# Kernel optimization log

Hardware: AMD Instinct MI355X
Metric: run time of the kernel (lower is better)

## Reference

```python
import jax, jax.numpy as jnp
import numpy as np


def setup_inputs() -> dict:
    key = jax.random.key(0)
    k1, k2, k3 = jax.random.split(key, 3)
    B, N, M, C = 4, 4096, 8192, 64
    PPU = 64.0  # points_per_unit
    xz = jax.random.normal(k1, (B, M, 1), dtype=jnp.float32) * 10.0  # grid locations
    z = jax.random.normal(k2, (B, C, M), dtype=jnp.float32)          # channels-first features
    x = jax.random.normal(k3, (B, N, 1), dtype=jnp.float32) * 10.0   # query locations
    log_scale = jnp.asarray(np.log(2.0 / PPU), dtype=jnp.float32)
    return {"xz": xz, "z": z, "x": x, "log_scale": log_scale}


def reference(xz, z, x, log_scale):
    # pairwise squared distances between x [B,N,1] and xz [B,M,1] -> [B,N,M]
    diff = x - jnp.swapaxes(xz, -1, -2)            # [B,N,M]
    dists2 = diff * diff
    # RBF weights (no normalization)
    weights = jnp.exp(-0.5 * dists2 / jnp.exp(2.0 * log_scale))  # [B,N,M]
    # z: [B,C,M] -> transpose -> [B,M,C]; weights @ z^T -> [B,N,C]
    out = jnp.einsum('bnm,bcm->bnc', weights, z)
    return out
```

## Files before the change

### kernel.cpp

```cpp
#include <hip/hip_runtime.h>
#include <math.h>

#define B 4
#define N 4096
#define M 8192
#define C 64
#define NB 2048
#define XMIN (-64.0f)
#define INV_BW 16.0f
#define CUT 10.0f
#define QG 16
#define NSUBP 4
#define NSUBQ 2

typedef __attribute__((ext_vector_type(8))) short short8;
typedef __attribute__((ext_vector_type(4))) float f32x4;

__device__ __forceinline__ int bucket_of(float v) {
    int k = (int)floorf((v - XMIN) * INV_BW);
    return min(max(k, 0), NB - 1);
}

__device__ __forceinline__ unsigned short f2bf(float f) {
    unsigned int u = __float_as_uint(f);
    return (unsigned short)((u + 0x7FFF + ((u >> 16) & 1)) >> 16);
}

__global__ __launch_bounds__(1024) void prep_kernel(
    const float* __restrict__ xz, const float* __restrict__ x,
    const float* __restrict__ z,
    int* __restrict__ part,
    unsigned short* __restrict__ zt)
{
    const int t   = threadIdx.x;
    const int blk = blockIdx.x;

    __shared__ int   h[NB];
    __shared__ float tile[64][65];

    if (blk < 24) {
        h[t] = 0; h[t + 1024] = 0;
        __syncthreads();
        const bool isQ = blk >= 16;
        const int  b   = isQ ? (blk - 16) >> 1 : blk >> 2;
        const int  sub = isQ ? (blk - 16) & 1  : blk & 3;
        const float* src = (isQ ? x + b * N : xz + b * M) + sub * 2048;
        float2 v2 = *(const float2*)(src + t * 2);
        atomicAdd(&h[bucket_of(v2.x)], 1);
        atomicAdd(&h[bucket_of(v2.y)], 1);
        __syncthreads();
        part[blk * NB + t]        = h[t];
        part[blk * NB + 1024 + t] = h[1024 + t];
    } else {
        const int tix = blk - 24;
        const int b   = tix >> 7;
        const int m0  = (tix & 127) * 64;
        const int m   = t & 63;
        #pragma unroll
        for (int k = 0; k < 4; ++k) {
            int c = (t >> 6) + 16 * k;
            tile[c][m] = z[((size_t)b * C + c) * M + m0 + m];
        }
        __syncthreads();
        const int j  = t >> 4;
        const int c4 = t & 15;
        ushort4 v4;
        v4.x = f2bf(tile[c4 * 4 + 0][j]);
        v4.y = f2bf(tile[c4 * 4 + 1][j]);
        v4.z = f2bf(tile[c4 * 4 + 2][j]);
        v4.w = f2bf(tile[c4 * 4 + 3][j]);
        ((ushort4*)zt)[((size_t)b * M + m0 + j) * 16 + c4] = v4;
    }
}

__global__ __launch_bounds__(256) void scat_kernel(
    const float* __restrict__ xz, const float* __restrict__ x,
    const int* __restrict__ part,
    int* __restrict__ bucket_start,
    float* __restrict__ xs,
    int* __restrict__ iord,
    float* __restrict__ qcs,
    int* __restrict__ qis)
{
    const int t    = threadIdx.x;
    const int lane = t & 63;
    const int w    = t >> 6;
    const int bid  = blockIdx.x;
    const bool isQ = bid >= 16;
    const int  b   = isQ ? (bid - 16) >> 1 : bid >> 2;
    const int  sub = isQ ? (bid - 16) & 1  : bid & 3;
    const int  nsub = isQ ? NSUBQ : NSUBP;
    const int  pb0  = isQ ? 16 + b * 2 : b * 4;
    const float* src = (isQ ? x + b * N : xz + b * M) + sub * 2048;

    __shared__ int base[NB];
    __shared__ int cnt[NB];
    __shared__ int wsum[4];

    int tot[8], mine[8];
    #pragma unroll
    for (int j = 0; j < 8; ++j) { tot[j] = 0; mine[j] = 0; }
    for (int s_ = 0; s_ < nsub; ++s_) {
        #pragma unroll
        for (int j = 0; j < 8; ++j) {
            const int v = part[(pb0 + s_) * NB + t * 8 + j];
            tot[j] += v;
            if (s_ < sub) mine[j] += v;
        }
    }
    int pre[8]; int tsum = 0;
    #pragma unroll
    for (int j = 0; j < 8; ++j) { pre[j] = tsum; tsum += tot[j]; }
    int s = tsum;
    #pragma unroll
    for (int off = 1; off < 64; off <<= 1) {
        int up = __shfl_up(s, off, 64);
        if (lane >= off) s += up;
    }
    if (lane == 63) wsum[w] = s;
    #pragma unroll
    for (int i = 0; i < 8; ++i) cnt[t + 256 * i] = 0;
    __syncthreads();
    int woff = 0;
    for (int i = 0; i < w; ++i) woff += wsum[i];
    const int excl = woff + s - tsum;
    #pragma unroll
    for (int j = 0; j < 8; ++j) base[t * 8 + j] = excl + pre[j] + mine[j];
    if (!isQ && sub == 0) {
        #pragma unroll
        for (int j = 0; j < 8; ++j)
            bucket_start[b * (NB + 1) + t * 8 + j] = excl + pre[j];
        if (t == 255) bucket_start[b * (NB + 1) + NB] = woff + s;
    }
    __syncthreads();

    #pragma unroll
    for (int j = 0; j < 2; ++j) {
        float4 v4 = *(const float4*)(src + t * 4 + j * 1024);
        float vv[4] = {v4.x, v4.y, v4.z, v4.w};
        #pragma unroll
        for (int c = 0; c < 4; ++c) {
            const int k    = bucket_of(vv[c]);
            const int slot = base[k] + atomicAdd(&cnt[k], 1);
            const int orig = sub * 2048 + t * 4 + j * 1024 + c;
            if (!isQ) {
                xs[b * M + slot]   = vv[c];
                iord[b * M + slot] = orig;
            } else {
                qcs[b * N + slot] = vv[c];
                qis[b * N + slot] = orig;
            }
        }
    }
}

__global__ __launch_bounds__(256) void gather_kernel(
    const float* __restrict__ log_scale,
    const int* __restrict__ bucket_start,
    const float* __restrict__ xs,
    const float* __restrict__ qcs,
    const int* __restrict__ qis,
    const int* __restrict__ iord,
    const unsigned short* __restrict__ zt,
    float* __restrict__ out)
{
    const int t    = threadIdx.x;
    const int lane = t & 63;
    const int w    = t >> 6;
    const int quad = lane >> 4;
    const int low4 = lane & 15;
    const int g  = blockIdx.x;
    const int b  = g >> 8;
    const int g0 = (g & 255) * QG;

    __shared__ unsigned short zr[64 * 64];
    __shared__ unsigned short wl[QG][72];
    __shared__ float qcS[QG];
    __shared__ int   qiS[QG];

    const float ls   = log_scale[0];
    const float coef = -0.5f * __expf(-2.0f * ls);
    const float R    = sqrtf(CUT / (-coef));

    if (t < QG) {
        qcS[t] = qcs[b * N + g0 + t];
        qiS[t] = qis[b * N + g0 + t];
    }
    __syncthreads();

    float xmin = qcS[0], xmax = qcS[0];
    #pragma unroll
    for (int j = 1; j < QG; ++j) {
        xmin = fminf(xmin, qcS[j]);
        xmax = fmaxf(xmax, qcS[j]);
    }
    const int s0 = bucket_start[b * (NB + 1) + bucket_of(xmin - R)];
    const int s1 = bucket_start[b * (NB + 1) + bucket_of(xmax + R) + 1];
    const int e0 = s0 & ~63;
    const int e1 = (s1 + 63) & ~63;

    const int qw = w * 4 + (lane >> 4);
    const int pg = lane & 15;
    const float qv = qcS[qw];

    f32x4 acc = {0.f, 0.f, 0.f, 0.f};

    const float* xsb = xs + b * M;
    const int* iordb = iord + b * M;
    const unsigned short* ztb = zt + (size_t)b * M * C;

    for (int cs = e0; cs < e1; cs += 64) {
        __syncthreads();
        #pragma unroll
        for (int r = 0; r < 2; ++r) {
            const int ridx = (w * 2 + r) * 8 + (lane >> 3);
            const int gm   = iordb[cs + ridx];
            const unsigned short* gp = ztb + (size_t)gm * C + (lane & 7) * 8;
            unsigned short* lp = zr + (w * 2 + r) * 512;
            __builtin_amdgcn_global_load_lds(
                (const __attribute__((address_space(1))) void*)gp,
                (__attribute__((address_space(3))) void*)lp, 16, 0, 0);
        }
        {
            const float4 xp4 = *(const float4*)(xsb + cs + pg * 4);
            float d0 = qv - xp4.x, d1 = qv - xp4.y;
            float d2 = qv - xp4.z, d3 = qv - xp4.w;
            ushort4 wv;
            wv.x = f2bf(__expf(coef * d0 * d0));
            wv.y = f2bf(__expf(coef * d1 * d1));
            wv.z = f2bf(__expf(coef * d2 * d2));
            wv.w = f2bf(__expf(coef * d3 * d3));
            *(ushort4*)&wl[qw][pg * 4] = wv;
        }
        __syncthreads();
        #pragma unroll
        for (int kh = 0; kh < 2; ++kh) {
            short8 afrag = *(const short8*)&wl[low4][kh * 32 + quad * 8];
            short8 bfrag;
            #pragma unroll
            for (int j = 0; j < 8; ++j) {
                const int p = kh * 32 + quad * 8 + j;
                bfrag[j] = (short)zr[p * 64 + w * 16 + low4];
            }
            acc = __builtin_amdgcn_mfma_f32_16x16x32_bf16(afrag, bfrag, acc, 0, 0, 0);
        }
    }

    #pragma unroll
    for (int r = 0; r < 4; ++r) {
        const int q = quad * 4 + r;
        out[((size_t)b * N + qiS[q]) * C + w * 16 + low4] = acc[r];
    }
}

extern "C" void kernel_launch(void* const* d_in, const int* in_sizes, int n_in,
                              void* d_out, int out_size, void* d_ws, size_t ws_size,
                              hipStream_t stream) {
    const float* xz = (const float*)d_in[0];
    const float* z  = (const float*)d_in[1];
    const float* x  = (const float*)d_in[2];
    const float* ls = (const float*)d_in[3];
    float* out = (float*)d_out;

    char* ws = (char*)d_ws;
    size_t off = 0;
    auto alloc = [&](size_t bytes) { void* p = ws + off; off += (bytes + 255) & ~size_t(255); return p; };

    unsigned short* zt = (unsigned short*)alloc((size_t)B * M * C * sizeof(unsigned short));
    float* xs   = (float*)alloc(((size_t)B * M + 64) * sizeof(float));
    int*   iord = (int*)alloc((size_t)B * M * sizeof(int));
    float* qcs  = (float*)alloc((size_t)B * N * sizeof(float));
    int*   qis  = (int*)alloc((size_t)B * N * sizeof(int));
    int*   bst  = (int*)alloc((size_t)B * (NB + 1) * sizeof(int));
    int*   part = (int*)alloc((size_t)24 * NB * sizeof(int));

    prep_kernel<<<536, 1024, 0, stream>>>(xz, x, z, part, zt);
    scat_kernel<<<24, 256, 0, stream>>>(xz, x, part, bst, xs, iord, qcs, qis);
    gather_kernel<<<B * (N / QG), 256, 0, stream>>>(ls, bst, xs, qcs, qis, iord, zt, out);
}
```

Measured before the change: 82.45 us.

## Prefetch next chunk's grid indices and positions; compute query range from sorted endpoints

Software-pipelines the per-chunk loads of grid indices and grid coordinates one iteration ahead, so the dependent gather address and the weight computation no longer wait on a global load at the top of each iteration. It also computes the query range from the first and last sorted query coordinates straight from global memory, before the first barrier, rather than scanning shared memory after a barrier. The bucket range is widened by one bucket on each side as a safety margin, which can add chunks of work. The new range logic assumes the queries are sorted within each group.

```diff
diff --git a/kernel.cpp b/kernel.cpp
--- a/kernel.cpp
+++ b/kernel.cpp
@@ -186,51 +186,66 @@
         qcS[t] = qcs[b * N + g0 + t];
         qiS[t] = qis[b * N + g0 + t];
     }
-    __syncthreads();
-
-    float xmin = qcS[0], xmax = qcS[0];
-    #pragma unroll
-    for (int j = 1; j < QG; ++j) {
-        xmin = fminf(xmin, qcS[j]);
-        xmax = fmaxf(xmax, qcS[j]);
-    }
-    const int s0 = bucket_start[b * (NB + 1) + bucket_of(xmin - R)];
-    const int s1 = bucket_start[b * (NB + 1) + bucket_of(xmax + R) + 1];
+
+    const float qlo = qcs[b * N + g0];
+    const float qhi = qcs[b * N + g0 + QG - 1];
+    const int k0 = max(bucket_of(qlo - R) - 1, 0);
+    const int k1 = min(bucket_of(qhi + R) + 1, NB - 1);
+    const int s0 = bucket_start[b * (NB + 1) + k0];
+    const int s1 = bucket_start[b * (NB + 1) + k1 + 1];
     const int e0 = s0 & ~63;
     const int e1 = (s1 + 63) & ~63;
 
-    const int qw = w * 4 + (lane >> 4);
-    const int pg = lane & 15;
-    const float qv = qcS[qw];
-
-    f32x4 acc = {0.f, 0.f, 0.f, 0.f};
+    const int qw = w * 4 + quad;
+    const int pg = low4;
 
     const float* xsb = xs + b * M;
     const int* iordb = iord + b * M;
     const unsigned short* ztb = zt + (size_t)b * M * C;
 
+    const int ridx0 = (w * 2 + 0) * 8 + (lane >> 3);
+    const int ridx1 = (w * 2 + 1) * 8 + (lane >> 3);
+    int gmA = 0, gmB = 0;
+    float4 xpA = {0.f, 0.f, 0.f, 0.f};
+    if (e0 < e1) {
+        gmA = iordb[e0 + ridx0];
+        gmB = iordb[e0 + ridx1];
+        xpA = *(const float4*)(xsb + e0 + pg * 4);
+    }
+
+    __syncthreads();
+    const float qv = qcS[qw];
+
+    f32x4 acc = {0.f, 0.f, 0.f, 0.f};
+
     for (int cs = e0; cs < e1; cs += 64) {
         __syncthreads();
-        #pragma unroll
-        for (int r = 0; r < 2; ++r) {
-            const int ridx = (w * 2 + r) * 8 + (lane >> 3);
-            const int gm   = iordb[cs + ridx];
-            const unsigned short* gp = ztb + (size_t)gm * C + (lane & 7) * 8;
-            unsigned short* lp = zr + (w * 2 + r) * 512;
+        {
+            const unsigned short* gpA = ztb + (size_t)gmA * C + (lane & 7) * 8;
+            const unsigned short* gpB = ztb + (size_t)gmB * C + (lane & 7) * 8;
             __builtin_amdgcn_global_load_lds(
-                (const __attribute__((address_space(1))) void*)gp,
-                (__attribute__((address_space(3))) void*)lp, 16, 0, 0);
+                (const __attribute__((address_space(1))) void*)gpA,
+                (__attribute__((address_space(3))) void*)(zr + (w * 2 + 0) * 512),
+                16, 0, 0);
+            __builtin_amdgcn_global_load_lds(
+                (const __attribute__((address_space(1))) void*)gpB,
+                (__attribute__((address_space(3))) void*)(zr + (w * 2 + 1) * 512),
+                16, 0, 0);
         }
         {
-            const float4 xp4 = *(const float4*)(xsb + cs + pg * 4);
-            float d0 = qv - xp4.x, d1 = qv - xp4.y;
-            float d2 = qv - xp4.z, d3 = qv - xp4.w;
+            float d0 = qv - xpA.x, d1 = qv - xpA.y;
+            float d2 = qv - xpA.z, d3 = qv - xpA.w;
             ushort4 wv;
             wv.x = f2bf(__expf(coef * d0 * d0));
             wv.y = f2bf(__expf(coef * d1 * d1));
             wv.z = f2bf(__expf(coef * d2 * d2));
             wv.w = f2bf(__expf(coef * d3 * d3));
             *(ushort4*)&wl[qw][pg * 4] = wv;
+        }
+        if (cs + 64 < e1) {
+            gmA = iordb[cs + 64 + ridx0];
+            gmB = iordb[cs + 64 + ridx1];
+            xpA = *(const float4*)(xsb + cs + 64 + pg * 4);
         }
         __syncthreads();
         #pragma unroll
```

Result: no change. 81.96 us (-0.6%).
